# Optimization experiments

Hardware: AMD Instinct MI355X
Metric: run time of the kernel (lower is better)

Reference implementation:

```python
import jax, jax.numpy as jnp
import numpy as np

B, T, C = 2, 2048, 1024
H, D = 16, 64


def setup_inputs() -> dict:
    key = jax.random.key(0)
    k1, k2, k3 = jax.random.split(key, 3)
    x = jax.random.normal(k1, (B, T, C), dtype=jnp.float32)
    w_qkv = jax.random.normal(k2, (C, 3 * H * D), dtype=jnp.float32) * (C ** -0.5)
    w_proj = jax.random.normal(k3, (H * D, C), dtype=jnp.float32) * ((H * D) ** -0.5)
    sink_logit = jnp.zeros((H,), dtype=jnp.float32)
    return {"x": x, "w_qkv": w_qkv, "w_proj": w_proj, "sink_logit": sink_logit}


def reference(x, w_qkv, w_proj, sink_logit):
    b, t, c = x.shape
    qkv = x @ w_qkv                                  # [B,T,3HD]
    q, k, v = jnp.split(qkv, 3, axis=-1)
    # [B,H,T,D]
    q = q.reshape(b, t, H, D).transpose(0, 2, 1, 3)
    k = k.reshape(b, t, H, D).transpose(0, 2, 1, 3)
    v = v.reshape(b, t, H, D).transpose(0, 2, 1, 3)

    scale = 1.0 / jnp.sqrt(jnp.asarray(D, dtype=x.dtype))
    scores = jnp.einsum('bhqd,bhkd->bhqk', q, k) * scale   # [B,H,T,T]
    neg_inf = jnp.finfo(x.dtype).min
    causal = jnp.tril(jnp.ones((t, t), dtype=bool))
    scores = jnp.where(causal[None, None], scores, neg_inf)

    # sink column: per-head learnable logit b (added post-scale, V is zero)
    sink = jnp.broadcast_to(sink_logit.reshape(1, H, 1, 1), (b, H, t, 1)).astype(x.dtype)
    aug = jnp.concatenate([sink, scores], axis=-1)          # [B,H,T,T+1]
    attn = jax.nn.softmax(aug, axis=-1)
    # sink V is zero, so drop the sink column for the value contraction
    y = jnp.einsum('bhqk,bhkd->bhqd', attn[..., 1:], v)     # [B,H,T,D]
    y = y.transpose(0, 2, 1, 3).reshape(b, t, H * D)
    return y @ w_proj
```

## Files before the change

### kernel.cpp

```cpp
#include <hip/hip_runtime.h>
#include <hip/hip_bf16.h>
#include <stdint.h>

#define B_ 2
#define T_ 2048
#define C_ 1024
#define H_ 16
#define D_ 64

typedef __attribute__((ext_vector_type(8))) short short8;
typedef __attribute__((ext_vector_type(4))) float floatx4;

__device__ __forceinline__ float bf2f(uint16_t b) {
    return __uint_as_float(((uint32_t)b) << 16);
}
__device__ __forceinline__ uint16_t f2b(float f) {
    __hip_bfloat16 h = __float2bfloat16(f);
    return *(uint16_t*)&h;
}
__device__ __forceinline__ void glds16(const uint16_t* g, uint16_t* l) {
    __builtin_amdgcn_global_load_lds(
        (const __attribute__((address_space(1))) uint32_t*)g,
        (__attribute__((address_space(3))) uint32_t*)l, 16, 0, 0);
}

__global__ void canon_x(const float* __restrict__ in, uint16_t* __restrict__ out,
                        int n) {
    int i = (blockIdx.x * 256 + threadIdx.x) * 4;
    if (i >= n) return;
    float4 v = *(const float4*)(in + i);
    out[i + 0] = f2b(v.x);
    out[i + 1] = f2b(v.y);
    out[i + 2] = f2b(v.z);
    out[i + 3] = f2b(v.w);
}

__global__ void transpose_conv(const float* __restrict__ in, uint16_t* __restrict__ out,
                               int R, int W) {
    __shared__ uint16_t tile[32][33];
    int tx = threadIdx.x, ty = threadIdx.y;
    int c0 = blockIdx.x * 32, r0 = blockIdx.y * 32;
    #pragma unroll
    for (int i = 0; i < 32; i += 8)
        tile[ty + i][tx] = f2b(in[(size_t)(r0 + ty + i) * W + (c0 + tx)]);
    __syncthreads();
    #pragma unroll
    for (int i = 0; i < 32; i += 8)
        out[(size_t)(c0 + ty + i) * R + (r0 + tx)] = tile[tx][ty + i];
}

template <bool OUT_F32>
__global__ __launch_bounds__(256)
void gemm_bt(const uint16_t* __restrict__ A, const uint16_t* __restrict__ Bt,
             void* __restrict__ Cv, int M, int N, int K) {
    __shared__ uint16_t As[128][32];
    __shared__ uint16_t Bs[128][32];
    int tid = threadIdx.x;
    int wave = tid >> 6, lane = tid & 63;
    int quad = lane >> 4, l16 = lane & 15;
    int wr = (wave >> 1) * 64, wc = (wave & 1) * 64;
    int row0 = blockIdx.x * 128, col0 = blockIdx.y * 128;

    int srow = wave * 32 + (lane >> 2);
    int scol = (lane & 3) * 8;
    const uint16_t* gA1 = A + (size_t)(row0 + srow) * K + scol;
    const uint16_t* gA2 = A + (size_t)(row0 + srow + 16) * K + scol;
    const uint16_t* gB1 = Bt + (size_t)(col0 + srow) * K + scol;
    const uint16_t* gB2 = Bt + (size_t)(col0 + srow + 16) * K + scol;
    uint16_t* lA1 = &As[srow][scol];
    uint16_t* lA2 = &As[srow + 16][scol];
    uint16_t* lB1 = &Bs[srow][scol];
    uint16_t* lB2 = &Bs[srow + 16][scol];

    floatx4 acc[4][4];
    #pragma unroll
    for (int i = 0; i < 4; i++)
        #pragma unroll
        for (int j = 0; j < 4; j++)
            acc[i][j] = (floatx4){0.f, 0.f, 0.f, 0.f};

    for (int k0 = 0; k0 < K; k0 += 32) {
        __syncthreads();
        glds16(gA1 + k0, lA1);
        glds16(gA2 + k0, lA2);
        glds16(gB1 + k0, lB1);
        glds16(gB2 + k0, lB2);
        __syncthreads();
        short8 af[4], bf[4];
        #pragma unroll
        for (int i = 0; i < 4; i++)
            af[i] = *(const short8*)&As[wr + i * 16 + l16][quad * 8];
        #pragma unroll
        for (int j = 0; j < 4; j++)
            bf[j] = *(const short8*)&Bs[wc + j * 16 + l16][quad * 8];
        #pragma unroll
        for (int i = 0; i < 4; i++)
            #pragma unroll
            for (int j = 0; j < 4; j++)
                acc[i][j] = __builtin_amdgcn_mfma_f32_16x16x32_bf16(
                    af[i], bf[j], acc[i][j], 0, 0, 0);
    }
    #pragma unroll
    for (int i = 0; i < 4; i++) {
        #pragma unroll
        for (int j = 0; j < 4; j++) {
            int rbase = row0 + wr + i * 16 + quad * 4;
            int cg = col0 + wc + j * 16 + l16;
            #pragma unroll
            for (int r = 0; r < 4; r++) {
                if (OUT_F32)
                    ((float*)Cv)[(size_t)(rbase + r) * N + cg] = acc[i][j][r];
                else
                    ((uint16_t*)Cv)[(size_t)(rbase + r) * N + cg] = f2b(acc[i][j][r]);
            }
        }
    }
}

__global__ __launch_bounds__(256, 2)
void attn_mfma(const uint16_t* __restrict__ qkv,
               const float* __restrict__ sink,
               uint16_t* __restrict__ y) {
    __shared__ uint16_t Ks[2][64][72];
    __shared__ uint16_t Vt[2][64][72];
    __shared__ uint16_t Pl[4][32][72];

    int tid = threadIdx.x;
    int w = tid >> 6, lane = tid & 63;
    int quad = lane >> 4, l16 = lane & 15;

    int id = blockIdx.x;
    int pair = id >> 5, bh = id & 31;
    int b = bh >> 4, h = bh & 15;
    int strip = (w < 2) ? (31 - pair) : pair;
    int q0w = strip * 64 + (w & 1) * 32;
    int ktiles = 32 - pair;
    int myktiles = strip + 1;

    const uint16_t* qkv_b = qkv + (size_t)b * T_ * 3072;

    short8 qf[2][2];
    #pragma unroll
    for (int qt = 0; qt < 2; qt++) {
        int qrow = q0w + qt * 16 + l16;
        #pragma unroll
        for (int kd = 0; kd < 2; kd++) {
            uint4 raw = *(const uint4*)(qkv_b + (size_t)qrow * 3072 + h * 64 +
                                        kd * 32 + quad * 8);
            const uint16_t* rp = (const uint16_t*)&raw;
            short8 f;
            #pragma unroll
            for (int j = 0; j < 8; j++)
                f[j] = (short)f2b(bf2f(rp[j]) * 0.125f);
            qf[qt][kd] = f;
        }
    }

    float m_s[2], l_s[2];
    m_s[0] = m_s[1] = sink[h];
    l_s[0] = l_s[1] = 1.0f;
    floatx4 acc_o[2][4];
    #pragma unroll
    for (int qt = 0; qt < 2; qt++)
        #pragma unroll
        for (int dt = 0; dt < 4; dt++)
            acc_o[qt][dt] = (floatx4){0.f, 0.f, 0.f, 0.f};

    int t2 = tid >> 3;
    int dg = tid & 7;
    const uint16_t* kgp = qkv_b + 1024 + h * 64 + (size_t)(2 * t2) * 3072 + dg * 8;
    const uint16_t* vgp = kgp + 1024;
    int vcw = 2 * (t2 ^ (4 * dg));

    uint4 kr0 = *(const uint4*)(kgp);
    uint4 kr1 = *(const uint4*)(kgp + 3072);
    uint4 vr0 = *(const uint4*)(vgp);
    uint4 vr1 = *(const uint4*)(vgp + 3072);
    {
        *(uint4*)&Ks[0][2 * t2][dg * 8] = kr0;
        *(uint4*)&Ks[0][2 * t2 + 1][dg * 8] = kr1;
        const uint16_t* a0 = (const uint16_t*)&vr0;
        const uint16_t* a1 = (const uint16_t*)&vr1;
        #pragma unroll
        for (int j = 0; j < 8; j++)
            *(uint32_t*)&Vt[0][dg * 8 + j][vcw] =
                (uint32_t)a0[j] | ((uint32_t)a1[j] << 16);
    }
    if (ktiles > 1) {
        kr0 = *(const uint4*)(kgp + 64 * 3072);
        kr1 = *(const uint4*)(kgp + 64 * 3072 + 3072);
        vr0 = *(const uint4*)(vgp + 64 * 3072);
        vr1 = *(const uint4*)(vgp + 64 * 3072 + 3072);
    }
    __syncthreads();

    for (int kt = 0; kt < ktiles; kt++) {
        int cur = kt & 1;
        if (kt + 1 < ktiles) {
            *(uint4*)&Ks[cur ^ 1][2 * t2][dg * 8] = kr0;
            *(uint4*)&Ks[cur ^ 1][2 * t2 + 1][dg * 8] = kr1;
            const uint16_t* a0 = (const uint16_t*)&vr0;
            const uint16_t* a1 = (const uint16_t*)&vr1;
            #pragma unroll
            for (int j = 0; j < 8; j++)
                *(uint32_t*)&Vt[cur ^ 1][dg * 8 + j][vcw] =
                    (uint32_t)a0[j] | ((uint32_t)a1[j] << 16);
        }
        if (kt + 2 < ktiles) {
            size_t off = (size_t)(kt + 2) * 64 * 3072;
            kr0 = *(const uint4*)(kgp + off);
            kr1 = *(const uint4*)(kgp + off + 3072);
            vr0 = *(const uint4*)(vgp + off);
            vr1 = *(const uint4*)(vgp + off + 3072);
        }
        if (kt < myktiles) {
            short8 kf[4][2];
            #pragma unroll
            for (int rt = 0; rt < 4; rt++) {
                kf[rt][0] = *(const short8*)&Ks[cur][rt * 16 + l16][quad * 8];
                kf[rt][1] = *(const short8*)&Ks[cur][rt * 16 + l16][32 + quad * 8];
            }
            short8 vf[2][4];
            #pragma unroll
            for (int kb = 0; kb < 2; kb++)
                #pragma unroll
                for (int dt = 0; dt < 4; dt++) {
                    int d = dt * 16 + l16;
                    int col = 2 * (((kb * 16) + quad * 4) ^ (4 * (d >> 3)));
                    vf[kb][dt] = *(const short8*)&Vt[cur][d][col];
                }
            #pragma unroll
            for (int qt = 0; qt < 2; qt++) {
                floatx4 acc_s[4];
                #pragma unroll
                for (int rt = 0; rt < 4; rt++)
                    acc_s[rt] = (floatx4){0.f, 0.f, 0.f, 0.f};
                #pragma unroll
                for (int rt = 0; rt < 4; rt++) {
                    acc_s[rt] = __builtin_amdgcn_mfma_f32_16x16x32_bf16(
                        kf[rt][0], qf[qt][0], acc_s[rt], 0, 0, 0);
                    acc_s[rt] = __builtin_amdgcn_mfma_f32_16x16x32_bf16(
                        kf[rt][1], qf[qt][1], acc_s[rt], 0, 0, 0);
                }
                if (kt == strip) {
                    int qg = q0w + qt * 16 + l16;
                    #pragma unroll
                    for (int rt = 0; rt < 4; rt++) {
                        int kg = kt * 64 + rt * 16 + quad * 4;
                        #pragma unroll
                        for (int r = 0; r < 4; r++)
                            if (kg + r > qg) acc_s[rt][r] = -1e30f;
                    }
                }
                float mx = -1e30f;
                #pragma unroll
                for (int rt = 0; rt < 4; rt++)
                    #pragma unroll
                    for (int r = 0; r < 4; r++) mx = fmaxf(mx, acc_s[rt][r]);
                mx = fmaxf(mx, __shfl_xor(mx, 16));
                mx = fmaxf(mx, __shfl_xor(mx, 32));
                float mnew = fmaxf(m_s[qt], mx);
                float alpha = __expf(m_s[qt] - mnew);
                m_s[qt] = mnew;
                float psum = 0.f;
                #pragma unroll
                for (int rt = 0; rt < 4; rt++) {
                    float p0 = __expf(acc_s[rt][0] - mnew);
                    float p1 = __expf(acc_s[rt][1] - mnew);
                    float p2 = __expf(acc_s[rt][2] - mnew);
                    float p3 = __expf(acc_s[rt][3] - mnew);
                    psum += (p0 + p1) + (p2 + p3);
                    uint2 pk;
                    pk.x = (uint32_t)f2b(p0) | ((uint32_t)f2b(p1) << 16);
                    pk.y = (uint32_t)f2b(p2) | ((uint32_t)f2b(p3) << 16);
                    *(uint2*)&Pl[w][qt * 16 + l16][rt * 16 + quad * 4] = pk;
                }
                psum += __shfl_xor(psum, 16);
                psum += __shfl_xor(psum, 32);
                l_s[qt] = l_s[qt] * alpha + psum;
                #pragma unroll
                for (int r = 0; r < 4; r++) {
                    float ar = __shfl(alpha, (lane & 48) | (quad * 4 + r));
                    #pragma unroll
                    for (int dt = 0; dt < 4; dt++) acc_o[qt][dt][r] *= ar;
                }
                #pragma unroll
                for (int kb = 0; kb < 2; kb++) {
                    short8 pf = *(const short8*)&Pl[w][qt * 16 + l16][kb * 32 + quad * 8];
                    #pragma unroll
                    for (int dt = 0; dt < 4; dt++)
                        acc_o[qt][dt] = __builtin_amdgcn_mfma_f32_16x16x32_bf16(
                            pf, vf[kb][dt], acc_o[qt][dt], 0, 0, 0);
                }
            }
        }
        __syncthreads();
    }

    #pragma unroll
    for (int qt = 0; qt < 2; qt++) {
        #pragma unroll
        for (int r = 0; r < 4; r++) {
            float lr = __shfl(l_s[qt], (lane & 48) | (quad * 4 + r));
            float inv = 1.0f / lr;
            int qg = q0w + qt * 16 + quad * 4 + r;
            uint16_t* yp = y + (size_t)(b * T_ + qg) * 1024 + h * 64;
            #pragma unroll
            for (int dt = 0; dt < 4; dt++)
                yp[dt * 16 + l16] = f2b(acc_o[qt][dt][r] * inv);
        }
    }
}

extern "C" void kernel_launch(void* const* d_in, const int* in_sizes, int n_in,
                              void* d_out, int out_size, void* d_ws, size_t ws_size,
                              hipStream_t stream) {
    const float* x      = (const float*)d_in[0];
    const float* w_qkv  = (const float*)d_in[1];
    const float* w_proj = (const float*)d_in[2];
    const float* sink   = (const float*)d_in[3];
    float* out          = (float*)d_out;

    char* ws = (char*)d_ws;
    uint16_t* wt_qkv  = (uint16_t*)ws;
    uint16_t* wt_proj = (uint16_t*)(ws + 6291456);
    uint16_t* x_c     = (uint16_t*)(ws + 8388608);
    uint16_t* qkv     = (uint16_t*)(ws + 16777216);
    uint16_t* yb      = (uint16_t*)(ws + 41943040);

    canon_x<<<4194304 / 1024, 256, 0, stream>>>(x, x_c, 4194304);
    transpose_conv<<<dim3(3072 / 32, 1024 / 32), dim3(32, 8), 0, stream>>>(
        w_qkv, wt_qkv, 1024, 3072);
    transpose_conv<<<dim3(1024 / 32, 1024 / 32), dim3(32, 8), 0, stream>>>(
        w_proj, wt_proj, 1024, 1024);

    gemm_bt<false><<<dim3(4096 / 128, 3072 / 128), 256, 0, stream>>>(
        x_c, wt_qkv, qkv, 4096, 3072, 1024);

    attn_mfma<<<dim3(16 * 32), 256, 0, stream>>>(qkv, sink, yb);

    gemm_bt<true><<<dim3(4096 / 128, 1024 / 128), 256, 0, stream>>>(
        yb, wt_proj, out, 4096, 1024, 1024);
}
```

Measured before the change: 201.4 us.

## Single-buffer attention LDS, regroup query blocks, raise occupancy, drop LDS-direct GEMM loads

The attention kernel now gives each block one contiguous 128-row query block instead of pairing a short and a long 64-row strip. Blocks are ordered longest-first across groups, and the causal mask check is generalised to the new layout. K/V shared memory goes from double to single buffering, which halves that LDS use, and launch bounds rise from 2 to 4 blocks per CU. In exchange, the loop now has two barriers per tile and keeps only a one-tile register prefetch. Separately, the GEMM replaces global_load_lds direct-to-LDS copies with register-staged uint4 loads issued before the barrier.

Measured after the change: 339.7 us. 1.69x slower.

```diff
diff --git a/kernel.cpp b/kernel.cpp
--- a/kernel.cpp
+++ b/kernel.cpp
@@ -17,11 +17,6 @@
 __device__ __forceinline__ uint16_t f2b(float f) {
     __hip_bfloat16 h = __float2bfloat16(f);
     return *(uint16_t*)&h;
-}
-__device__ __forceinline__ void glds16(const uint16_t* g, uint16_t* l) {
-    __builtin_amdgcn_global_load_lds(
-        (const __attribute__((address_space(1))) uint32_t*)g,
-        (__attribute__((address_space(3))) uint32_t*)l, 16, 0, 0);
 }
 
 __global__ void canon_x(const float* __restrict__ in, uint16_t* __restrict__ out,
@@ -60,17 +55,7 @@
     int quad = lane >> 4, l16 = lane & 15;
     int wr = (wave >> 1) * 64, wc = (wave & 1) * 64;
     int row0 = blockIdx.x * 128, col0 = blockIdx.y * 128;
-
-    int srow = wave * 32 + (lane >> 2);
-    int scol = (lane & 3) * 8;
-    const uint16_t* gA1 = A + (size_t)(row0 + srow) * K + scol;
-    const uint16_t* gA2 = A + (size_t)(row0 + srow + 16) * K + scol;
-    const uint16_t* gB1 = Bt + (size_t)(col0 + srow) * K + scol;
-    const uint16_t* gB2 = Bt + (size_t)(col0 + srow + 16) * K + scol;
-    uint16_t* lA1 = &As[srow][scol];
-    uint16_t* lA2 = &As[srow + 16][scol];
-    uint16_t* lB1 = &Bs[srow][scol];
-    uint16_t* lB2 = &Bs[srow + 16][scol];
+    int srow = tid >> 1, scol = (tid & 1) * 16;
 
     floatx4 acc[4][4];
     #pragma unroll
@@ -80,11 +65,15 @@
             acc[i][j] = (floatx4){0.f, 0.f, 0.f, 0.f};
 
     for (int k0 = 0; k0 < K; k0 += 32) {
+        const uint4* ga = (const uint4*)(A + (size_t)(row0 + srow) * K + k0 + scol);
+        const uint4* gb = (const uint4*)(Bt + (size_t)(col0 + srow) * K + k0 + scol);
+        uint4 a0 = ga[0], a1 = ga[1];
+        uint4 b0 = gb[0], b1 = gb[1];
         __syncthreads();
-        glds16(gA1 + k0, lA1);
-        glds16(gA2 + k0, lA2);
-        glds16(gB1 + k0, lB1);
-        glds16(gB2 + k0, lB2);
+        *(uint4*)&As[srow][scol]     = a0;
+        *(uint4*)&As[srow][scol + 8] = a1;
+        *(uint4*)&Bs[srow][scol]     = b0;
+        *(uint4*)&Bs[srow][scol + 8] = b1;
         __syncthreads();
         short8 af[4], bf[4];
         #pragma unroll
@@ -117,12 +106,12 @@
     }
 }
 
-__global__ __launch_bounds__(256, 2)
+__global__ __launch_bounds__(256, 4)
 void attn_mfma(const uint16_t* __restrict__ qkv,
                const float* __restrict__ sink,
                uint16_t* __restrict__ y) {
-    __shared__ uint16_t Ks[2][64][72];
-    __shared__ uint16_t Vt[2][64][72];
+    __shared__ uint16_t Ks[64][72];
+    __shared__ uint16_t Vt[64][72];
     __shared__ uint16_t Pl[4][32][72];
 
     int tid = threadIdx.x;
@@ -130,12 +119,13 @@
     int quad = lane >> 4, l16 = lane & 15;
 
     int id = blockIdx.x;
-    int pair = id >> 5, bh = id & 31;
+    int bh = id & 31;
+    int g = id >> 5;
+    int qb = (g < 8) ? (15 - g) : (g - 8);
     int b = bh >> 4, h = bh & 15;
-    int strip = (w < 2) ? (31 - pair) : pair;
-    int q0w = strip * 64 + (w & 1) * 32;
-    int ktiles = 32 - pair;
-    int myktiles = strip + 1;
+    int q0w = qb * 128 + w * 32;
+    int ktiles = 2 * qb + 2;
+    int myktiles = 2 * qb + 1 + (w >> 1);
 
     const uint16_t* qkv_b = qkv + (size_t)b * T_ * 3072;
 
@@ -176,125 +166,108 @@
     uint4 kr1 = *(const uint4*)(kgp + 3072);
     uint4 vr0 = *(const uint4*)(vgp);
     uint4 vr1 = *(const uint4*)(vgp + 3072);
-    {
-        *(uint4*)&Ks[0][2 * t2][dg * 8] = kr0;
-        *(uint4*)&Ks[0][2 * t2 + 1][dg * 8] = kr1;
-        const uint16_t* a0 = (const uint16_t*)&vr0;
-        const uint16_t* a1 = (const uint16_t*)&vr1;
-        #pragma unroll
-        for (int j = 0; j < 8; j++)
-            *(uint32_t*)&Vt[0][dg * 8 + j][vcw] =
-                (uint32_t)a0[j] | ((uint32_t)a1[j] << 16);
-    }
-    if (ktiles > 1) {
-        kr0 = *(const uint4*)(kgp + 64 * 3072);
-        kr1 = *(const uint4*)(kgp + 64 * 3072 + 3072);
-        vr0 = *(const uint4*)(vgp + 64 * 3072);
-        vr1 = *(const uint4*)(vgp + 64 * 3072 + 3072);
-    }
-    __syncthreads();
 
     for (int kt = 0; kt < ktiles; kt++) {
-        int cur = kt & 1;
-        if (kt + 1 < ktiles) {
-            *(uint4*)&Ks[cur ^ 1][2 * t2][dg * 8] = kr0;
-            *(uint4*)&Ks[cur ^ 1][2 * t2 + 1][dg * 8] = kr1;
+        __syncthreads();
+        *(uint4*)&Ks[2 * t2][dg * 8] = kr0;
+        *(uint4*)&Ks[2 * t2 + 1][dg * 8] = kr1;
+        {
             const uint16_t* a0 = (const uint16_t*)&vr0;
             const uint16_t* a1 = (const uint16_t*)&vr1;
             #pragma unroll
             for (int j = 0; j < 8; j++)
-                *(uint32_t*)&Vt[cur ^ 1][dg * 8 + j][vcw] =
+                *(uint32_t*)&Vt[dg * 8 + j][vcw] =
                     (uint32_t)a0[j] | ((uint32_t)a1[j] << 16);
         }
-        if (kt + 2 < ktiles) {
-            size_t off = (size_t)(kt + 2) * 64 * 3072;
+        __syncthreads();
+        if (kt + 1 < ktiles) {
+            size_t off = (size_t)(kt + 1) * 64 * 3072;
             kr0 = *(const uint4*)(kgp + off);
             kr1 = *(const uint4*)(kgp + off + 3072);
             vr0 = *(const uint4*)(vgp + off);
             vr1 = *(const uint4*)(vgp + off + 3072);
         }
-        if (kt < myktiles) {
-            short8 kf[4][2];
+        if (kt >= myktiles) continue;
+
+        short8 kf[4][2];
+        #pragma unroll
+        for (int rt = 0; rt < 4; rt++) {
+            kf[rt][0] = *(const short8*)&Ks[rt * 16 + l16][quad * 8];
+            kf[rt][1] = *(const short8*)&Ks[rt * 16 + l16][32 + quad * 8];
+        }
+        short8 vf[2][4];
+        #pragma unroll
+        for (int kb = 0; kb < 2; kb++)
+            #pragma unroll
+            for (int dt = 0; dt < 4; dt++) {
+                int d = dt * 16 + l16;
+                int col = 2 * (((kb * 16) + quad * 4) ^ (4 * (d >> 3)));
+                vf[kb][dt] = *(const short8*)&Vt[d][col];
+            }
+        #pragma unroll
+        for (int qt = 0; qt < 2; qt++) {
+            floatx4 acc_s[4];
+            #pragma unroll
+            for (int rt = 0; rt < 4; rt++)
+                acc_s[rt] = (floatx4){0.f, 0.f, 0.f, 0.f};
             #pragma unroll
             for (int rt = 0; rt < 4; rt++) {
-                kf[rt][0] = *(const short8*)&Ks[cur][rt * 16 + l16][quad * 8];
-                kf[rt][1] = *(const short8*)&Ks[cur][rt * 16 + l16][32 + quad * 8];
-            }
-            short8 vf[2][4];
-            #pragma unroll
-            for (int kb = 0; kb < 2; kb++)
-                #pragma unroll
-                for (int dt = 0; dt < 4; dt++) {
-                    int d = dt * 16 + l16;
-                    int col = 2 * (((kb * 16) + quad * 4) ^ (4 * (d >> 3)));
-                    vf[kb][dt] = *(const short8*)&Vt[cur][d][col];
-                }
-            #pragma unroll
-            for (int qt = 0; qt < 2; qt++) {
-                floatx4 acc_s[4];
-                #pragma unroll
-                for (int rt = 0; rt < 4; rt++)
-                    acc_s[rt] = (floatx4){0.f, 0.f, 0.f, 0.f};
+                acc_s[rt] = __builtin_amdgcn_mfma_f32_16x16x32_bf16(
+                    kf[rt][0], qf[qt][0], acc_s[rt], 0, 0, 0);
+                acc_s[rt] = __builtin_amdgcn_mfma_f32_16x16x32_bf16(
+                    kf[rt][1], qf[qt][1], acc_s[rt], 0, 0, 0);
+            }
+            if (kt * 64 + 63 > q0w) {
+                int qg = q0w + qt * 16 + l16;
                 #pragma unroll
                 for (int rt = 0; rt < 4; rt++) {
-                    acc_s[rt] = __builtin_amdgcn_mfma_f32_16x16x32_bf16(
-                        kf[rt][0], qf[qt][0], acc_s[rt], 0, 0, 0);
-                    acc_s[rt] = __builtin_amdgcn_mfma_f32_16x16x32_bf16(
-                        kf[rt][1], qf[qt][1], acc_s[rt], 0, 0, 0);
+                    int kg = kt * 64 + rt * 16 + quad * 4;
+                    #pragma unroll
+                    for (int r = 0; r < 4; r++)
+                        if (kg + r > qg) acc_s[rt][r] = -1e30f;
                 }
-                if (kt == strip) {
-                    int qg = q0w + qt * 16 + l16;
-                    #pragma unroll
-                    for (int rt = 0; rt < 4; rt++) {
-                        int kg = kt * 64 + rt * 16 + quad * 4;
-                        #pragma unroll
-                        for (int r = 0; r < 4; r++)
-                            if (kg + r > qg) acc_s[rt][r] = -1e30f;
-                    }
-                }
-                float mx = -1e30f;
+            }
+            float mx = -1e30f;
+            #pragma unroll
+            for (int rt = 0; rt < 4; rt++)
                 #pragma unroll
-                for (int rt = 0; rt < 4; rt++)
-                    #pragma unroll
-                    for (int r = 0; r < 4; r++) mx = fmaxf(mx, acc_s[rt][r]);
-                mx = fmaxf(mx, __shfl_xor(mx, 16));
-                mx = fmaxf(mx, __shfl_xor(mx, 32));
-                float mnew = fmaxf(m_s[qt], mx);
-                float alpha = __expf(m_s[qt] - mnew);
-                m_s[qt] = mnew;
-                float psum = 0.f;
+                for (int r = 0; r < 4; r++) mx = fmaxf(mx, acc_s[rt][r]);
+            mx = fmaxf(mx, __shfl_xor(mx, 16));
+            mx = fmaxf(mx, __shfl_xor(mx, 32));
+            float mnew = fmaxf(m_s[qt], mx);
+            float alpha = __expf(m_s[qt] - mnew);
+            m_s[qt] = mnew;
+            float psum = 0.f;
+            #pragma unroll
+            for (int rt = 0; rt < 4; rt++) {
+                float p0 = __expf(acc_s[rt][0] - mnew);
+                float p1 = __expf(acc_s[rt][1] - mnew);
+                float p2 = __expf(acc_s[rt][2] - mnew);
+                float p3 = __expf(acc_s[rt][3] - mnew);
+                psum += (p0 + p1) + (p2 + p3);
+                uint2 pk;
+                pk.x = (uint32_t)f2b(p0) | ((uint32_t)f2b(p1) << 16);
+                pk.y = (uint32_t)f2b(p2) | ((uint32_t)f2b(p3) << 16);
+                *(uint2*)&Pl[w][qt * 16 + l16][rt * 16 + quad * 4] = pk;
+            }
+            psum += __shfl_xor(psum, 16);
+            psum += __shfl_xor(psum, 32);
+            l_s[qt] = l_s[qt] * alpha + psum;
+            #pragma unroll
+            for (int r = 0; r < 4; r++) {
+                float ar = __shfl(alpha, (lane & 48) | (quad * 4 + r));
                 #pragma unroll
-                for (int rt = 0; rt < 4; rt++) {
-                    float p0 = __expf(acc_s[rt][0] - mnew);
-                    float p1 = __expf(acc_s[rt][1] - mnew);
-                    float p2 = __expf(acc_s[rt][2] - mnew);
-                    float p3 = __expf(acc_s[rt][3] - mnew);
-                    psum += (p0 + p1) + (p2 + p3);
-                    uint2 pk;
-                    pk.x = (uint32_t)f2b(p0) | ((uint32_t)f2b(p1) << 16);
-                    pk.y = (uint32_t)f2b(p2) | ((uint32_t)f2b(p3) << 16);
-                    *(uint2*)&Pl[w][qt * 16 + l16][rt * 16 + quad * 4] = pk;
-                }
-                psum += __shfl_xor(psum, 16);
-                psum += __shfl_xor(psum, 32);
-                l_s[qt] = l_s[qt] * alpha + psum;
+                for (int dt = 0; dt < 4; dt++) acc_o[qt][dt][r] *= ar;
+            }
+            #pragma unroll
+            for (int kb = 0; kb < 2; kb++) {
+                short8 pf = *(const short8*)&Pl[w][qt * 16 + l16][kb * 32 + quad * 8];
                 #pragma unroll
-                for (int r = 0; r < 4; r++) {
-                    float ar = __shfl(alpha, (lane & 48) | (quad * 4 + r));
-                    #pragma unroll
-                    for (int dt = 0; dt < 4; dt++) acc_o[qt][dt][r] *= ar;
-                }
-                #pragma unroll
-                for (int kb = 0; kb < 2; kb++) {
-                    short8 pf = *(const short8*)&Pl[w][qt * 16 + l16][kb * 32 + quad * 8];
-                    #pragma unroll
-                    for (int dt = 0; dt < 4; dt++)
-                        acc_o[qt][dt] = __builtin_amdgcn_mfma_f32_16x16x32_bf16(
-                            pf, vf[kb][dt], acc_o[qt][dt], 0, 0, 0);
-                }
-            }
-        }
-        __syncthreads();
+                for (int dt = 0; dt < 4; dt++)
+                    acc_o[qt][dt] = __builtin_amdgcn_mfma_f32_16x16x32_bf16(
+                        pf, vf[kb][dt], acc_o[qt][dt], 0, 0, 0);
+            }
+        }
     }
 
     #pragma unroll
```
